# Performance work log

Measured on AMD Instinct MI355X. Metric: run time of the kernel, lower is better.

## Reference

```python
import jax, jax.numpy as jnp
import numpy as np


def setup_inputs() -> dict:
    key = jax.random.key(0)
    k1, k2, k3, k4 = jax.random.split(key, 4)
    B, n_env, in_ch, out_ch, code_ch, modes1, L = 16, 8, 32, 32, 16, 64, 8192
    scale = 1.0 / (in_ch * out_ch)
    return {
        "x": jax.random.normal(k1, (B, n_env * in_ch, L), dtype=jnp.float32),
        "codes": jax.random.normal(k2, (n_env, code_ch), dtype=jnp.float32),
        "com_weights": scale * jax.random.uniform(k3, (in_ch, out_ch, modes1, 2), dtype=jnp.float32),
        "code_weights": scale * jax.random.uniform(k4, (code_ch * in_ch, out_ch, modes1, 2), dtype=jnp.float32),
        "filter_weights": -3.0 * jnp.ones((modes1,), dtype=jnp.float32),
    }


def _as_complex(w):
    return w[..., 0] + 1j * w[..., 1]


def reference(x, codes, com_weights, code_weights, filter_weights):
    B, C, L = x.shape
    n_env, code_ch = codes.shape
    in_ch = C // n_env
    out_ch = com_weights.shape[1]
    modes1 = com_weights.shape[2]
    n_freq = L // 2 + 1

    # FFT and reshape to [B, e, i, freq]
    x_ft = jnp.fft.rfft(x).reshape(B, n_env, in_ch, n_freq)
    xm = x_ft[..., :modes1]  # mode truncation

    cw = _as_complex(com_weights)  # [i, o, m]
    codew = _as_complex(code_weights.reshape(code_ch, in_ch, out_ch, modes1, 2))  # [c,i,o,m]
    env_w = jnp.einsum('ec,ciom->eiom', codes.astype(codew.dtype), codew)

    # hardsigmoid(filter_weights): clip(x/6 + 0.5, 0, 1)
    lam = jnp.clip(filter_weights / 6.0 + 0.5, 0.0, 1.0)  # [m]

    out_m = (lam * jnp.einsum('beim,iom->beom', xm, cw)
             + (1.0 - lam) * jnp.einsum('beim,eiom->beom', xm, env_w))  # [B,e,o,m]

    # zero-pad back to full spectrum then inverse FFT
    out_ft = jnp.zeros((B, n_env, out_ch, n_freq), dtype=out_m.dtype)
    out_ft = out_ft.at[..., :modes1].set(out_m)
    out_ft = out_ft.reshape(B, n_env * out_ch, n_freq)
    return jnp.fft.irfft(out_ft, n=L)
```

## Files before the change

### kernel.cpp

```cpp
#include <hip/hip_runtime.h>
#include <hip/hip_bf16.h>
#include <math.h>
#include <stdint.h>

typedef __bf16 bf16_t;
typedef __bf16 bf16x8 __attribute__((ext_vector_type(8)));
typedef float  f32x4  __attribute__((ext_vector_type(4)));
typedef _Float16 f16x4 __attribute__((ext_vector_type(4)));

#define L_LEN 8192
#define MODES 64
#define NCOMP 128
#define M_ROWS 4096
#define SPLITS 16

__device__ __forceinline__ void g2lds16(const void* g, void* l) {
  __builtin_amdgcn_global_load_lds(
      (__attribute__((address_space(1))) void*)(uintptr_t)(g),
      (__attribute__((address_space(3))) void*)(l), 16, 0, 0);
}

__global__ __launch_bounds__(256) void prep(bf16_t* __restrict__ B1t,
                                            bf16_t* __restrict__ B1,
                                            const float* __restrict__ codes,
                                            const float* __restrict__ comw,
                                            const float* __restrict__ codew,
                                            const float* __restrict__ fw,
                                            float* __restrict__ W) {
  const float C0 = 7.6699039394282061e-4f;
  if (blockIdx.x < 512) {
    const int id = blockIdx.x * 256 + threadIdx.x;
    if (id < 65536) {
      const int l8 = id & 1023, k = id >> 10;
      const int l0 = l8 * 8;
      bf16x8 vc, vs;
#pragma unroll
      for (int j = 0; j < 8; ++j) {
        int r = ((l0 + j) * k) & (L_LEN - 1);
        float s, c;
        __sincosf((float)r * C0, &s, &c);
        vc[j] = (bf16_t)c;
        vs[j] = (bf16_t)(-s);
      }
      *(bf16x8*)(B1t + (size_t)k * L_LEN + l0)           = vc;
      *(bf16x8*)(B1t + (size_t)(MODES + k) * L_LEN + l0) = vs;
    } else {
      const int id2 = id - 65536;
      const int k8 = id2 & 7, l = id2 >> 3;
      const int kk = k8 * 8;
      bf16x8 vc, vs;
#pragma unroll
      for (int j = 0; j < 8; ++j) {
        int r = (l * (kk + j)) & (L_LEN - 1);
        float s, c;
        __sincosf((float)r * C0, &s, &c);
        vc[j] = (bf16_t)c;
        vs[j] = (bf16_t)(-s);
      }
      *(bf16x8*)(B1 + (size_t)l * NCOMP + kk)         = vc;
      *(bf16x8*)(B1 + (size_t)l * NCOMP + MODES + kk) = vs;
    }
  } else {
    int id = (blockIdx.x - 512) * 256 + threadIdx.x;
    int kp = id & 31;
    int o = (id >> 5) & 31;
    int i = (id >> 10) & 31;
    int e = id >> 15;
    float lam0 = fminf(fmaxf(fw[2 * kp]     * (1.0f / 6.0f) + 0.5f, 0.0f), 1.0f);
    float lam1 = fminf(fmaxf(fw[2 * kp + 1] * (1.0f / 6.0f) + 0.5f, 0.0f), 1.0f);
    f32x4 a = (f32x4){0.f, 0.f, 0.f, 0.f};
#pragma unroll
    for (int c = 0; c < 16; ++c) {
      float cd = codes[e * 16 + c];
      f32x4 p = *(const f32x4*)(codew + ((((c * 32 + i) * 32 + o) * 64) << 1) + kp * 4);
      a += cd * p;
    }
    f32x4 q = *(const f32x4*)(comw + (((i * 32 + o) * 64) << 1) + kp * 4);
    f32x4 r;
    r[0] = lam0 * q[0] + (1.f - lam0) * a[0];
    r[1] = lam0 * q[1] + (1.f - lam0) * a[1];
    r[2] = lam1 * q[2] + (1.f - lam1) * a[2];
    r[3] = lam1 * q[3] + (1.f - lam1) * a[3];
    *(f32x4*)(W + ((((e * 32 + i) * 32 + o) * 64) << 1) + kp * 4) = r;
  }
}

__global__ __launch_bounds__(256, 4) void stage1(const float* __restrict__ x,
                                                 const bf16_t* __restrict__ B1t,
                                                 _Float16* __restrict__ Xp) {
  __shared__ bf16_t Bs[2][128 * 64];
  const int t = threadIdx.x;
  const int lane = t & 63;
  const int w = t >> 6;
  const int l15 = lane & 15, lq = lane >> 4;
  const int m0 = blockIdx.x * 64 + w * 16;
  const int k0 = blockIdx.y * 512;

  const float* aptr = x + (size_t)(m0 + l15) * L_LEN + k0 + lq * 8;

#pragma unroll
  for (int q = 0; q < 4; ++q) {
    int slot = t + 256 * q;
    int n = slot >> 3, m8 = slot & 7, j8 = m8 ^ (n & 7);
    g2lds16(B1t + (size_t)n * L_LEN + k0 + j8 * 8, (char*)(&Bs[0][0]) + slot * 16);
  }
  float4 pa0 = *(const float4*)(aptr + 0);
  float4 pa1 = *(const float4*)(aptr + 4);
  float4 pa2 = *(const float4*)(aptr + 32);
  float4 pa3 = *(const float4*)(aptr + 36);

  f32x4 acc[8];
#pragma unroll
  for (int nf = 0; nf < 8; ++nf) acc[nf] = (f32x4){0.f, 0.f, 0.f, 0.f};

#pragma unroll
  for (int ch = 0; ch < 8; ++ch) {
    float4 a0 = pa0, a1 = pa1, a2 = pa2, a3 = pa3;
    if (ch < 7) {
#pragma unroll
      for (int q = 0; q < 4; ++q) {
        int slot = t + 256 * q;
        int n = slot >> 3, m8 = slot & 7, j8 = m8 ^ (n & 7);
        g2lds16(B1t + (size_t)n * L_LEN + k0 + (ch + 1) * 64 + j8 * 8,
                (char*)(&Bs[(ch + 1) & 1][0]) + slot * 16);
      }
      const float* ap2 = aptr + (ch + 1) * 64;
      pa0 = *(const float4*)(ap2 + 0);
      pa1 = *(const float4*)(ap2 + 4);
      pa2 = *(const float4*)(ap2 + 32);
      pa3 = *(const float4*)(ap2 + 36);
      asm volatile("s_waitcnt vmcnt(8)" ::: "memory");
    } else {
      asm volatile("s_waitcnt vmcnt(0)" ::: "memory");
    }
    __builtin_amdgcn_s_barrier();
    asm volatile("" ::: "memory");
    bf16x8 av0 = {(bf16_t)a0.x, (bf16_t)a0.y, (bf16_t)a0.z, (bf16_t)a0.w,
                  (bf16_t)a1.x, (bf16_t)a1.y, (bf16_t)a1.z, (bf16_t)a1.w};
    bf16x8 av1 = {(bf16_t)a2.x, (bf16_t)a2.y, (bf16_t)a2.z, (bf16_t)a2.w,
                  (bf16_t)a3.x, (bf16_t)a3.y, (bf16_t)a3.z, (bf16_t)a3.w};
    const bf16_t* bb = &Bs[ch & 1][0];
    __builtin_amdgcn_s_setprio(1);
#pragma unroll
    for (int s = 0; s < 2; ++s) {
      bf16x8 av = s ? av1 : av0;
#pragma unroll
      for (int nf = 0; nf < 8; ++nf) {
        int n = nf * 16 + l15;
        int j8 = (s * 4 + lq) ^ (n & 7);
        bf16x8 bv = *(const bf16x8*)(bb + n * 64 + j8 * 8);
        acc[nf] = __builtin_amdgcn_mfma_f32_16x16x32_bf16(bv, av, acc[nf], 0, 0, 0);
      }
    }
    __builtin_amdgcn_s_setprio(0);
    if (ch < 7) __builtin_amdgcn_s_barrier();
  }

  _Float16* xout = Xp + (size_t)blockIdx.y * (M_ROWS * NCOMP) +
                   (size_t)(m0 + l15) * NCOMP + lq * 4;
#pragma unroll
  for (int nf = 0; nf < 8; ++nf)
    *(f16x4*)(xout + nf * 16) = (f16x4){(_Float16)acc[nf][0], (_Float16)acc[nf][1],
                                        (_Float16)acc[nf][2], (_Float16)acc[nf][3]};
}

__global__ __launch_bounds__(256) void mixk(const _Float16* __restrict__ Xp,
                                            const float* __restrict__ W,
                                            bf16_t* __restrict__ A2) {
  __shared__ __align__(16) float Xs[32 * 64];
  const int t = threadIdx.x;
  const int be = blockIdx.x;
  const int kh = blockIdx.y;
  const int e = be & 7;
  const int cb = kh * 32;
  const _Float16* xb = Xp + (size_t)be * (32 * NCOMP);
#pragma unroll
  for (int j = 0; j < 2; ++j) {
    int qid = t + 256 * j;
    int row = qid >> 4, sub = qid & 15;
    int col  = (sub < 8) ? (cb + sub * 4) : (64 + cb + (sub - 8) * 4);
    int scol = (sub < 8) ? (sub * 4)      : (32 + (sub - 8) * 4);
    f32x4 s = (f32x4){0.f, 0.f, 0.f, 0.f};
#pragma unroll
    for (int sp = 0; sp < 16; ++sp) {
      f16x4 v = *(const f16x4*)(xb + (size_t)sp * (M_ROWS * NCOMP) + row * NCOMP + col);
      s[0] += (float)v[0]; s[1] += (float)v[1]; s[2] += (float)v[2]; s[3] += (float)v[3];
    }
    *(f32x4*)(Xs + row * 64 + scol) = s;
  }
  __syncthreads();
  const int kb = t & 31;
  const int k = cb + kb;
  const int grp = t >> 5;
  float yre[4], yim[4];
#pragma unroll
  for (int j = 0; j < 4; ++j) { yre[j] = 0.f; yim[j] = 0.f; }
  for (int i = 0; i < 32; ++i) {
    float xr = Xs[i * 64 + kb];
    float xi = Xs[i * 64 + 32 + kb];
    const float* wp = W + ((((e * 32 + i) * 32 + grp * 4) * 64 + k) << 1);
#pragma unroll
    for (int j = 0; j < 4; ++j) {
      float2 wv = *(const float2*)(wp + j * 128);
      yre[j] += xr * wv.x - xi * wv.y;
      yim[j] += xr * wv.y + xi * wv.x;
    }
  }
  float sc = (k == 0) ? (1.0f / 8192.0f) : (2.0f / 8192.0f);
#pragma unroll
  for (int j = 0; j < 4; ++j) {
    int m = be * 32 + grp * 4 + j;
    A2[m * NCOMP + k]         = (bf16_t)(yre[j] * sc);
    A2[m * NCOMP + MODES + k] = (bf16_t)(yim[j] * sc);
  }
}

__global__ __launch_bounds__(256) void stage2(const bf16_t* __restrict__ A2,
                                              const bf16_t* __restrict__ B1,
                                              float* __restrict__ out) {
  __shared__ bf16_t Bs[128 * 128];
  const int t = threadIdx.x;
  const int lane = t & 63;
  const int w = t >> 6;
  const int l15 = lane & 15, lq = lane >> 4;
  const int m0 = blockIdx.x * 64 + w * 16;
  const int l0 = blockIdx.y * 128;

#pragma unroll
  for (int q = 0; q < 8; ++q) {
    int slot = t + 256 * q;
    int lr = slot >> 4, m16 = slot & 15, j8 = m16 ^ (lr & 15);
    g2lds16(B1 + (size_t)(l0 + lr) * NCOMP + j8 * 8, (char*)Bs + slot * 16);
  }
  const bf16_t* ap = A2 + (size_t)(m0 + l15) * NCOMP + lq * 8;
  bf16x8 av[4];
#pragma unroll
  for (int s = 0; s < 4; ++s) av[s] = *(const bf16x8*)(ap + s * 32);

  f32x4 acc[8];
#pragma unroll
  for (int nf = 0; nf < 8; ++nf) acc[nf] = (f32x4){0.f, 0.f, 0.f, 0.f};

  __syncthreads();

  __builtin_amdgcn_s_setprio(1);
#pragma unroll
  for (int s = 0; s < 4; ++s) {
#pragma unroll
    for (int nf = 0; nf < 8; ++nf) {
      int lr = nf * 16 + l15;
      int j8 = (s * 4 + lq) ^ (lr & 15);
      bf16x8 bv = *(const bf16x8*)(Bs + lr * 128 + j8 * 8);
      acc[nf] = __builtin_amdgcn_mfma_f32_16x16x32_bf16(bv, av[s], acc[nf], 0, 0, 0);
    }
  }
  __builtin_amdgcn_s_setprio(0);

  float* op = out + (size_t)(m0 + l15) * L_LEN + l0 + lq * 4;
#pragma unroll
  for (int nf = 0; nf < 8; ++nf)
    *(float4*)(op + nf * 16) = (float4){acc[nf][0], acc[nf][1], acc[nf][2], acc[nf][3]};
}

extern "C" void kernel_launch(void* const* d_in, const int* in_sizes, int n_in,
                              void* d_out, int out_size, void* d_ws, size_t ws_size,
                              hipStream_t stream) {
  const float* x     = (const float*)d_in[0];
  const float* codes = (const float*)d_in[1];
  const float* comw  = (const float*)d_in[2];
  const float* codew = (const float*)d_in[3];
  const float* fw    = (const float*)d_in[4];
  float* out = (float*)d_out;
  char* ws = (char*)d_ws;
  bf16_t*   B1t = (bf16_t*)(ws);
  bf16_t*   B1  = (bf16_t*)(ws + (size_t)(2u << 20));
  float*    W   = (float*) (ws + (size_t)(4u << 20));
  bf16_t*   A2  = (bf16_t*)(ws + (size_t)(20u << 20));
  _Float16* Xp  = (_Float16*)(ws + (size_t)(24u << 20));

  prep<<<1536, 256, 0, stream>>>(B1t, B1, codes, comw, codew, fw, W);
  stage1<<<dim3(64, SPLITS), 256, 0, stream>>>(x, B1t, Xp);
  mixk<<<dim3(128, 2), 256, 0, stream>>>(Xp, W, A2);
  stage2<<<dim3(64, 64), 256, 0, stream>>>(A2, B1, out);
}
```

Baseline: 290.3 us.

## Deepen stage1 pipeline to triple-buffered LDS and halve split-K count

Stage1 now stages B tiles into three LDS buffers and keeps A loads two chunks ahead, giving more memory latency hiding per block. Each block covers 1024 K elements instead of 512, so only 8 split-K partials are written and then summed in mixk. This cuts partial-sum traffic, but it uses more LDS, lowers occupancy (launch bounds 2 instead of 4) and launches half as many blocks. The host launch grid presumably must change to match; it is not shown.

Measured after the change: 299.3 us. +3.1%, slower.

```diff
diff --git a/kernel.cpp b/kernel.cpp
--- a/kernel.cpp
+++ b/kernel.cpp
@@ -12,7 +12,8 @@
 #define MODES 64
 #define NCOMP 128
 #define M_ROWS 4096
-#define SPLITS 16
+#define SPLITS 8
+#define NCH 16
 
 __device__ __forceinline__ void g2lds16(const void* g, void* l) {
   __builtin_amdgcn_global_load_lds(
@@ -85,50 +86,55 @@
   }
 }
 
-__global__ __launch_bounds__(256, 4) void stage1(const float* __restrict__ x,
+__global__ __launch_bounds__(256, 2) void stage1(const float* __restrict__ x,
                                                  const bf16_t* __restrict__ B1t,
                                                  _Float16* __restrict__ Xp) {
-  __shared__ bf16_t Bs[2][128 * 64];
+  __shared__ bf16_t Bs[3][128 * 64];
   const int t = threadIdx.x;
   const int lane = t & 63;
   const int w = t >> 6;
   const int l15 = lane & 15, lq = lane >> 4;
   const int m0 = blockIdx.x * 64 + w * 16;
-  const int k0 = blockIdx.y * 512;
+  const int k0 = blockIdx.y * 1024;
 
   const float* aptr = x + (size_t)(m0 + l15) * L_LEN + k0 + lq * 8;
 
-#pragma unroll
-  for (int q = 0; q < 4; ++q) {
-    int slot = t + 256 * q;
-    int n = slot >> 3, m8 = slot & 7, j8 = m8 ^ (n & 7);
-    g2lds16(B1t + (size_t)n * L_LEN + k0 + j8 * 8, (char*)(&Bs[0][0]) + slot * 16);
-  }
-  float4 pa0 = *(const float4*)(aptr + 0);
-  float4 pa1 = *(const float4*)(aptr + 4);
-  float4 pa2 = *(const float4*)(aptr + 32);
-  float4 pa3 = *(const float4*)(aptr + 36);
-
+#define STAGE_B(CH)                                                            \
+  {                                                                            \
+    _Pragma("unroll")                                                          \
+    for (int q = 0; q < 4; ++q) {                                              \
+      int slot = t + 256 * q;                                                  \
+      int n = slot >> 3, m8 = slot & 7, j8 = m8 ^ (n & 7);                     \
+      g2lds16(B1t + (size_t)n * L_LEN + k0 + (CH) * 64 + j8 * 8,               \
+              (char*)(&Bs[(CH) % 3][0]) + slot * 16);                          \
+    }                                                                          \
+  }
+#define LOAD_A(CH, SET)                                                        \
+  {                                                                            \
+    const float* ap_ = aptr + (CH) * 64;                                       \
+    pa[SET][0] = *(const float4*)(ap_ + 0);                                    \
+    pa[SET][1] = *(const float4*)(ap_ + 4);                                    \
+    pa[SET][2] = *(const float4*)(ap_ + 32);                                   \
+    pa[SET][3] = *(const float4*)(ap_ + 36);                                   \
+  }
+
+  float4 pa[2][4];
   f32x4 acc[8];
 #pragma unroll
   for (int nf = 0; nf < 8; ++nf) acc[nf] = (f32x4){0.f, 0.f, 0.f, 0.f};
 
-#pragma unroll
-  for (int ch = 0; ch < 8; ++ch) {
-    float4 a0 = pa0, a1 = pa1, a2 = pa2, a3 = pa3;
-    if (ch < 7) {
-#pragma unroll
-      for (int q = 0; q < 4; ++q) {
-        int slot = t + 256 * q;
-        int n = slot >> 3, m8 = slot & 7, j8 = m8 ^ (n & 7);
-        g2lds16(B1t + (size_t)n * L_LEN + k0 + (ch + 1) * 64 + j8 * 8,
-                (char*)(&Bs[(ch + 1) & 1][0]) + slot * 16);
-      }
-      const float* ap2 = aptr + (ch + 1) * 64;
-      pa0 = *(const float4*)(ap2 + 0);
-      pa1 = *(const float4*)(ap2 + 4);
-      pa2 = *(const float4*)(ap2 + 32);
-      pa3 = *(const float4*)(ap2 + 36);
+  STAGE_B(0); LOAD_A(0, 0);
+  STAGE_B(1); LOAD_A(1, 1);
+
+#pragma unroll
+  for (int ch = 0; ch < NCH; ++ch) {
+    float4 a0 = pa[ch & 1][0], a1 = pa[ch & 1][1],
+           a2 = pa[ch & 1][2], a3 = pa[ch & 1][3];
+    if (ch < NCH - 2) {
+      STAGE_B(ch + 2);
+      LOAD_A(ch + 2, ch & 1);
+      asm volatile("s_waitcnt vmcnt(16)" ::: "memory");
+    } else if (ch == NCH - 2) {
       asm volatile("s_waitcnt vmcnt(8)" ::: "memory");
     } else {
       asm volatile("s_waitcnt vmcnt(0)" ::: "memory");
@@ -139,7 +145,7 @@
                   (bf16_t)a1.x, (bf16_t)a1.y, (bf16_t)a1.z, (bf16_t)a1.w};
     bf16x8 av1 = {(bf16_t)a2.x, (bf16_t)a2.y, (bf16_t)a2.z, (bf16_t)a2.w,
                   (bf16_t)a3.x, (bf16_t)a3.y, (bf16_t)a3.z, (bf16_t)a3.w};
-    const bf16_t* bb = &Bs[ch & 1][0];
+    const bf16_t* bb = &Bs[ch % 3][0];
     __builtin_amdgcn_s_setprio(1);
 #pragma unroll
     for (int s = 0; s < 2; ++s) {
@@ -153,8 +159,10 @@
       }
     }
     __builtin_amdgcn_s_setprio(0);
-    if (ch < 7) __builtin_amdgcn_s_barrier();
-  }
+    if (ch < NCH - 1) __builtin_amdgcn_s_barrier();
+  }
+#undef STAGE_B
+#undef LOAD_A
 
   _Float16* xout = Xp + (size_t)blockIdx.y * (M_ROWS * NCOMP) +
                    (size_t)(m0 + l15) * NCOMP + lq * 4;
@@ -182,7 +190,7 @@
     int scol = (sub < 8) ? (sub * 4)      : (32 + (sub - 8) * 4);
     f32x4 s = (f32x4){0.f, 0.f, 0.f, 0.f};
 #pragma unroll
-    for (int sp = 0; sp < 16; ++sp) {
+    for (int sp = 0; sp < SPLITS; ++sp) {
       f16x4 v = *(const f16x4*)(xb + (size_t)sp * (M_ROWS * NCOMP) + row * NCOMP + col);
       s[0] += (float)v[0]; s[1] += (float)v[1]; s[2] += (float)v[2]; s[3] += (float)v[3];
     }
```
